# Performance work log

Hardware: AMD Instinct MI355X
Metric: run time of the kernel (lower is better)

Reference implementation:

```python
import jax, jax.numpy as jnp
import numpy as np

N_NODES = 100000
N_EDGES = 1600000
IN_CH = 128
OUT_CH = 128
BN_EPS = 1e-5


def setup_inputs() -> dict:
    key = jax.random.key(0)
    ks = jax.random.split(key, 8)
    x = jax.random.normal(ks[0], (N_NODES, IN_CH), dtype=jnp.float32)
    edge_index = jax.random.randint(ks[1], (2, N_EDGES), 0, N_NODES, dtype=jnp.int32)
    s1 = 1.0 / np.sqrt(IN_CH)
    s2 = 1.0 / np.sqrt(OUT_CH)
    W1 = jax.random.uniform(ks[2], (IN_CH, OUT_CH), minval=-s1, maxval=s1, dtype=jnp.float32)
    b1 = jax.random.uniform(ks[3], (OUT_CH,), minval=-s1, maxval=s1, dtype=jnp.float32)
    gamma = jnp.ones((OUT_CH,), dtype=jnp.float32)
    beta = jnp.zeros((OUT_CH,), dtype=jnp.float32)
    W2 = jax.random.uniform(ks[4], (OUT_CH, OUT_CH), minval=-s2, maxval=s2, dtype=jnp.float32)
    b2 = jax.random.uniform(ks[5], (OUT_CH,), minval=-s2, maxval=s2, dtype=jnp.float32)
    return {"x": x, "edge_index": edge_index, "W1": W1, "b1": b1,
            "gamma": gamma, "beta": beta, "W2": W2, "b2": b2}


def reference(x, edge_index, W1, b1, gamma, beta, W2, b2):
    # GINConv (eps=0): h_i = x_i + sum_{(j->i) in E} x_j
    src, dst = edge_index[0], edge_index[1]
    agg = jax.ops.segment_sum(x[src], dst, num_segments=N_NODES)  # [N, in_ch]
    h = x + agg
    # MLP: Linear -> BatchNorm1d (training-mode batch stats) -> ReLU -> Linear -> ReLU
    h = h @ W1 + b1                                   # [N, out_ch]
    mean = jnp.mean(h, axis=0)
    var = jnp.mean(jnp.square(h - mean), axis=0)      # biased variance, as in BN training
    h = (h - mean) * jax.lax.rsqrt(var + BN_EPS) * gamma + beta
    h = jax.nn.relu(h)
    h = h @ W2 + b2
    return jax.nn.relu(h)
```

## Files before the change

### kernel.cpp

```cpp
#include <hip/hip_runtime.h>
#include <hip/hip_bf16.h>
#include <hip/hip_fp16.h>
#include <stdint.h>

#define CH 128
#define NCHUNK 512
#define MAXBKT 2048

typedef _Float16 f16x8 __attribute__((ext_vector_type(8)));
typedef float f32x4 __attribute__((ext_vector_type(4)));

static __device__ __forceinline__ float4 ld4(const float* p) {
    return *reinterpret_cast<const float4*>(p);
}

__global__ void k_bhist(const int* __restrict__ dst, int* __restrict__ H,
                        int nE, int nbkt, int chunkSz) {
    __shared__ int hist[MAXBKT];
    int c = blockIdx.x, tid = threadIdx.x;
    for (int i = tid; i < nbkt; i += 256) hist[i] = 0;
    __syncthreads();
    int s = c * chunkSz, e = min(s + chunkSz, nE);
    for (int i = s + tid; i < e; i += 256) atomicAdd(&hist[dst[i] >> 6], 1);
    __syncthreads();
    for (int i = tid; i < nbkt; i += 256) H[c * nbkt + i] = hist[i];
}

__global__ void k_btot(const int* __restrict__ H, int* __restrict__ T, int nchunk, int nbkt) {
    __shared__ int sd[256];
    int b = blockIdx.x, tid = threadIdx.x;
    int v = 0;
    for (int c = tid; c < nchunk; c += 256) v += H[c * nbkt + b];
    sd[tid] = v;
    __syncthreads();
    for (int o = 128; o > 0; o >>= 1) {
        if (tid < o) sd[tid] += sd[tid + o];
        __syncthreads();
    }
    if (tid == 0) T[b] = sd[0];
}

__global__ __launch_bounds__(1024) void k_bscan(const int* __restrict__ T,
                                                int* __restrict__ base, int nbkt) {
    __shared__ int ps[1024];
    int t = threadIdx.x;
    int a0 = (2 * t < nbkt) ? T[2 * t] : 0;
    int a1 = (2 * t + 1 < nbkt) ? T[2 * t + 1] : 0;
    ps[t] = a0 + a1;
    __syncthreads();
    for (int d = 1; d < 1024; d <<= 1) {
        int v = (t >= d) ? ps[t - d] : 0;
        __syncthreads();
        ps[t] += v;
        __syncthreads();
    }
    int excl = t ? ps[t - 1] : 0;
    if (2 * t < nbkt) base[2 * t] = excl;
    if (2 * t + 1 < nbkt) base[2 * t + 1] = excl + a0;
    if (t == 0) base[nbkt] = ps[1023];
}

__global__ __launch_bounds__(512) void k_boff(int* H, const int* __restrict__ base,
                                              int nchunk, int nbkt) {
    __shared__ int sd[NCHUNK];
    int b = blockIdx.x, t = threadIdx.x;
    int v = (t < nchunk) ? H[t * nbkt + b] : 0;
    sd[t] = v;
    __syncthreads();
    for (int d = 1; d < NCHUNK; d <<= 1) {
        int tv = (t >= d) ? sd[t - d] : 0;
        __syncthreads();
        sd[t] += tv;
        __syncthreads();
    }
    if (t < nchunk) H[t * nbkt + b] = base[b] + sd[t] - v;
}

__global__ void k_bscatter(const int* __restrict__ src, const int* __restrict__ dst,
                           const int* __restrict__ H, int* __restrict__ sorted,
                           int nE, int nbkt, int chunkSz) {
    __shared__ int cur[MAXBKT];
    int c = blockIdx.x, tid = threadIdx.x;
    for (int i = tid; i < nbkt; i += 256) cur[i] = H[c * nbkt + i];
    __syncthreads();
    int s = c * chunkSz, e = min(s + chunkSz, nE);
    for (int i = s + tid; i < e; i += 256) {
        int d = dst[i];
        int pos = atomicAdd(&cur[d >> 6], 1);
        sorted[pos] = src[i] | ((d & 63) << 17);
    }
}

__global__ __launch_bounds__(256) void k_bsort2(const int* __restrict__ sorted,
        const int* __restrict__ base, int* __restrict__ csr, int* __restrict__ offs,
        int n, int nbkt, int nE) {
    __shared__ int hist[64];
    __shared__ int cur[64];
    int b = blockIdx.x, tid = threadIdx.x;
    if (tid < 64) hist[tid] = 0;
    __syncthreads();
    int s = base[b], e = base[b + 1];
    for (int i = s + tid; i < e; i += 256)
        atomicAdd(&hist[(sorted[i] >> 17) & 63], 1);
    __syncthreads();
    if (tid < 64) {
        int h0 = hist[tid];
        int v = h0;
        for (int d = 1; d < 64; d <<= 1) {
            int t = __shfl_up(v, d, 64);
            if (tid >= d) v += t;
        }
        int excl = base[b] + v - h0;
        int node = b * 64 + tid;
        if (node < n) offs[node] = excl;
        cur[tid] = excl;
    }
    if (b == 0 && tid == 0) offs[n] = nE;
    __syncthreads();
    for (int i = s + tid; i < e; i += 256) {
        int p = sorted[i];
        int pos = atomicAdd(&cur[(p >> 17) & 63], 1);
        csr[pos] = p & 0x1FFFF;
    }
}

__global__ void k_tofp16(const float* __restrict__ x, uint32_t* __restrict__ xh, int n8) {
    int i = blockIdx.x * blockDim.x + threadIdx.x;
    int st = gridDim.x * blockDim.x;
    for (; i < n8; i += st) {
        float4 v0 = ld4(x + (size_t)i * 8);
        float4 v1 = ld4(x + (size_t)i * 8 + 4);
        __half2 h0 = __floats2half2_rn(v0.x, v0.y);
        __half2 h1 = __floats2half2_rn(v0.z, v0.w);
        __half2 h2 = __floats2half2_rn(v1.x, v1.y);
        __half2 h3 = __floats2half2_rn(v1.z, v1.w);
        uint4 o;
        o.x = *reinterpret_cast<unsigned*>(&h0);
        o.y = *reinterpret_cast<unsigned*>(&h1);
        o.z = *reinterpret_cast<unsigned*>(&h2);
        o.w = *reinterpret_cast<unsigned*>(&h3);
        reinterpret_cast<uint4*>(xh)[i] = o;
    }
}

static __device__ __forceinline__ void acc4(float4& a, uint2 v) {
    __half2 p0 = *reinterpret_cast<__half2*>(&v.x);
    __half2 p1 = *reinterpret_cast<__half2*>(&v.y);
    float2 f0 = __half22float2(p0), f1 = __half22float2(p1);
    a.x += f0.x; a.y += f0.y; a.z += f1.x; a.w += f1.y;
}

__global__ void k_aggregate_h2(const uint2* __restrict__ xv,
        const int* __restrict__ csr, const int* __restrict__ offs,
        uint2* __restrict__ h16, int n) {
    int wid = (blockIdx.x * blockDim.x + threadIdx.x) >> 6;
    int lane = threadIdx.x & 63;
    int nw = (gridDim.x * blockDim.x) >> 6;
    int hf = lane >> 5;
    int l32 = lane & 31;
    for (int node = wid; node < n; node += nw) {
        float4 a0 = make_float4(0.f, 0.f, 0.f, 0.f), a1 = a0, a2 = a0, a3 = a0;
        if (hf == 0) acc4(a0, xv[(size_t)node * 32 + l32]);
        int s = offs[node], e = offs[node + 1];
        int i = s + hf;
        for (; i + 6 < e; i += 8) {
            int e0 = csr[i], e1 = csr[i + 2], e2 = csr[i + 4], e3 = csr[i + 6];
            uint2 v0 = xv[(size_t)e0 * 32 + l32];
            uint2 v1 = xv[(size_t)e1 * 32 + l32];
            uint2 v2 = xv[(size_t)e2 * 32 + l32];
            uint2 v3 = xv[(size_t)e3 * 32 + l32];
            acc4(a0, v0); acc4(a1, v1); acc4(a2, v2); acc4(a3, v3);
        }
        for (; i < e; i += 2)
            acc4(a0, xv[(size_t)csr[i] * 32 + l32]);
        a0.x += a1.x + a2.x + a3.x;
        a0.y += a1.y + a2.y + a3.y;
        a0.z += a1.z + a2.z + a3.z;
        a0.w += a1.w + a2.w + a3.w;
        a0.x += __shfl_xor(a0.x, 32, 64);
        a0.y += __shfl_xor(a0.y, 32, 64);
        a0.z += __shfl_xor(a0.z, 32, 64);
        a0.w += __shfl_xor(a0.w, 32, 64);
        if (hf == 0) {
            __half2 o0 = __floats2half2_rn(a0.x, a0.y);
            __half2 o1 = __floats2half2_rn(a0.z, a0.w);
            uint2 ov;
            ov.x = *reinterpret_cast<unsigned*>(&o0);
            ov.y = *reinterpret_cast<unsigned*>(&o1);
            h16[(size_t)node * 32 + l32] = ov;
        }
    }
}

__global__ __launch_bounds__(256) void k_mgemm(
        const _Float16* __restrict__ A, const float* __restrict__ W,
        const float* __restrict__ bias, _Float16* __restrict__ O16,
        float* __restrict__ O32, float* __restrict__ stats,
        const float* __restrict__ bnsc, int nrows, int doStats) {
    __shared__ _Float16 WT[CH * CH];
    __shared__ float sc_sh[2 * CH];
    int tid = threadIdx.x;
    for (int idx4 = tid * 4; idx4 < CH * CH; idx4 += 1024) {
        float4 wv = ld4(W + idx4);
        int k = idx4 >> 7, col = idx4 & 127;
        int s = k >> 3, j = k & 7;
#pragma unroll
        for (int q = 0; q < 4; ++q) {
            int c = col + q;
            WT[c * CH + ((s ^ (c & 7)) << 3) + j] =
                (_Float16)(q == 0 ? wv.x : q == 1 ? wv.y : q == 2 ? wv.z : wv.w);
        }
    }
    if (bnsc && tid < 2 * CH) sc_sh[tid] = bnsc[tid];
    __syncthreads();

    int wv = tid >> 6, lane = tid & 63;
    int lr = lane & 15;
    int lg = lane >> 4;

    float bv[8];
#pragma unroll
    for (int ct = 0; ct < 8; ++ct) bv[ct] = bias[ct * 16 + lr];
    float ssum[8], ssq[8];
#pragma unroll
    for (int ct = 0; ct < 8; ++ct) { ssum[ct] = 0.f; ssq[ct] = 0.f; }

    int nchunks = (nrows + 63) >> 6;
    for (int chunk = blockIdx.x; chunk < nchunks; chunk += gridDim.x) {
        int row0 = chunk * 64 + wv * 16;
        int arow = min(row0 + lr, nrows - 1);
        const _Float16* Ap = A + (size_t)arow * CH + lg * 8;
        f16x8 a[4];
#pragma unroll
        for (int kb = 0; kb < 4; ++kb)
            a[kb] = *reinterpret_cast<const f16x8*>(Ap + kb * 32);
        if (bnsc) {
#pragma unroll
            for (int kb = 0; kb < 4; ++kb) {
                int k0 = kb * 32 + lg * 8;
#pragma unroll
                for (int j = 0; j < 8; ++j) {
                    float f = (float)a[kb][j];
                    f = fmaxf(fmaf(f, sc_sh[k0 + j], sc_sh[CH + k0 + j]), 0.f);
                    a[kb][j] = (_Float16)f;
                }
            }
        }

        f32x4 acc[8];
#pragma unroll
        for (int ct = 0; ct < 8; ++ct) acc[ct] = (f32x4){0.f, 0.f, 0.f, 0.f};
#pragma unroll
        for (int ct = 0; ct < 8; ++ct) {
            int col = ct * 16 + lr;
            const _Float16* Wp = &WT[col * CH];
            int sw = (col & 7) << 3;
#pragma unroll
            for (int kb = 0; kb < 4; ++kb) {
                int s = kb * 4 + lg;
                f16x8 b = *reinterpret_cast<const f16x8*>(Wp + ((s << 3) ^ sw));
                acc[ct] = __builtin_amdgcn_mfma_f32_16x16x32_f16(a[kb], b, acc[ct], 0, 0, 0);
            }
        }

#pragma unroll
        for (int ct = 0; ct < 8; ++ct) {
            int col = ct * 16 + lr;
#pragma unroll
            for (int r = 0; r < 4; ++r) {
                int row = row0 + lg * 4 + r;
                if (row < nrows) {
                    float v = acc[ct][r] + bv[ct];
                    if (doStats) {
                        O16[(size_t)row * CH + col] = (_Float16)v;
                        ssum[ct] += v;
                        ssq[ct] += v * v;
                    } else {
                        O32[(size_t)row * CH + col] = fmaxf(v, 0.f);
                    }
                }
            }
        }
    }

    if (doStats) {
#pragma unroll
        for (int ct = 0; ct < 8; ++ct) {
            ssum[ct] += __shfl_xor(ssum[ct], 16, 64); ssum[ct] += __shfl_xor(ssum[ct], 32, 64);
            ssq[ct]  += __shfl_xor(ssq[ct], 16, 64);  ssq[ct]  += __shfl_xor(ssq[ct], 32, 64);
        }
        __syncthreads();
        float* red = (float*)WT;
        if (lg == 0) {
#pragma unroll
            for (int ct = 0; ct < 8; ++ct) {
                red[wv * 128 + ct * 16 + lr] = ssum[ct];
                red[512 + wv * 128 + ct * 16 + lr] = ssq[ct];
            }
        }
        __syncthreads();
        if (tid < 128) {
            float s = 0.f, q = 0.f;
#pragma unroll
            for (int w = 0; w < 4; ++w) { s += red[w * 128 + tid]; q += red[512 + w * 128 + tid]; }
            atomicAdd(&stats[tid], s);
            atomicAdd(&stats[128 + tid], q);
        }
    }
}

__global__ void k_bnfin(const float* __restrict__ stats, const float* __restrict__ gamma,
        const float* __restrict__ beta, float* __restrict__ scsh, float invN) {
    int c = threadIdx.x;
    if (c < CH) {
        float mean = stats[c] * invN;
        float var = stats[CH + c] * invN - mean * mean;
        float sc = gamma[c] * rsqrtf(var + 1e-5f);
        scsh[c] = sc;
        scsh[CH + c] = beta[c] - mean * sc;
    }
}

extern "C" void kernel_launch(void* const* d_in, const int* in_sizes, int n_in,
                              void* d_out, int out_size, void* d_ws, size_t ws_size,
                              hipStream_t stream) {
    const float* x     = (const float*)d_in[0];
    const int*   ei    = (const int*)d_in[1];
    const float* W1    = (const float*)d_in[2];
    const float* b1    = (const float*)d_in[3];
    const float* gamma = (const float*)d_in[4];
    const float* beta  = (const float*)d_in[5];
    const float* W2    = (const float*)d_in[6];
    const float* b2    = (const float*)d_in[7];

    const int N = in_sizes[0] / CH;
    const int E = in_sizes[1] / 2;
    const int* esrc = ei;
    const int* edst = ei + E;
    const int nbkt = (N + 63) >> 6;
    const int chunkSz = (E + NCHUNK - 1) / NCHUNK;

    int* H      = (int*)d_out;
    int* sorted = (int*)((char*)d_out + (((size_t)NCHUNK * nbkt * 4 + 255) & ~(size_t)255));
    _Float16* h16 = (_Float16*)d_out;

    char* w = (char*)d_ws;
    auto take = [&](size_t bytes) {
        char* p = w;
        w += (bytes + 255) & ~(size_t)255;
        return p;
    };
    int*      csr    = (int*)take((size_t)E * 4);
    int*      T      = (int*)take((size_t)(nbkt + 1) * 4);
    int*      base   = (int*)take((size_t)(nbkt + 1) * 4);
    int*      offs   = (int*)take((size_t)(N + 1) * 4);
    float*    stats  = (float*)take(256 * 4);
    float*    scsh   = (float*)take(256 * 4);
    uint32_t* xh     = (uint32_t*)take((size_t)N * CH * 2);
    _Float16* h1     = (_Float16*)xh;

    hipMemsetAsync(stats, 0, 256 * 4, stream);

    k_bhist<<<NCHUNK, 256, 0, stream>>>(edst, H, E, nbkt, chunkSz);
    k_btot<<<nbkt, 256, 0, stream>>>(H, T, NCHUNK, nbkt);
    k_bscan<<<1, 1024, 0, stream>>>(T, base, nbkt);
    k_boff<<<nbkt, NCHUNK, 0, stream>>>(H, base, NCHUNK, nbkt);
    k_bscatter<<<NCHUNK, 256, 0, stream>>>(esrc, edst, H, sorted, E, nbkt, chunkSz);
    k_bsort2<<<nbkt, 256, 0, stream>>>(sorted, base, csr, offs, N, nbkt, E);
    k_tofp16<<<2048, 256, 0, stream>>>(x, xh, N * CH / 8);
    k_aggregate_h2<<<4096, 256, 0, stream>>>((const uint2*)xh, csr, offs,
                                             (uint2*)h16, N);
    k_mgemm<<<512, 256, 0, stream>>>(h16, W1, b1, h1, nullptr, stats, nullptr, N, 1);
    k_bnfin<<<1, 128, 0, stream>>>(stats, gamma, beta, scsh, 1.0f / (float)N);
    k_mgemm<<<512, 256, 0, stream>>>(h1, W2, b2, nullptr, (float*)d_out, nullptr, scsh, N, 0);
}
```

Baseline: 210.1 us.

## Fuse CSR build and fp16 conversion into one cooperative kernel with grid syncs

Replaces the seven preprocessing launches (fp16 conversion, bucket histogram, totals, scan, offsets, scatter, local sort) with a single cooperative kernel that uses grid-wide syncs between phases, falling back to the separate launches if the cooperative launch fails. The BN finalize kernel is folded into the second GEMM's prologue, and the aggregation gains a 16-edge unrolled loop for more loads in flight. The aim is to cut launch overhead and inter-kernel gaps, at the cost of grid.sync barriers and a scan bucket phase now run by only 512 blocks in a grid-stride loop.

```diff
diff --git a/kernel.cpp b/kernel.cpp
--- a/kernel.cpp
+++ b/kernel.cpp
@@ -1,8 +1,11 @@
 #include <hip/hip_runtime.h>
+#include <hip/hip_cooperative_groups.h>
 #include <hip/hip_bf16.h>
 #include <hip/hip_fp16.h>
 #include <stdint.h>
 
+namespace cg = cooperative_groups;
+
 #define CH 128
 #define NCHUNK 512
 #define MAXBKT 2048
@@ -14,6 +17,149 @@
     return *reinterpret_cast<const float4*>(p);
 }
 
+static __device__ __forceinline__ void cvt_store_fp16(uint32_t* xh, int i, float4 v0, float4 v1) {
+    __half2 h0 = __floats2half2_rn(v0.x, v0.y);
+    __half2 h1 = __floats2half2_rn(v0.z, v0.w);
+    __half2 h2 = __floats2half2_rn(v1.x, v1.y);
+    __half2 h3 = __floats2half2_rn(v1.z, v1.w);
+    uint4 o;
+    o.x = *reinterpret_cast<unsigned*>(&h0);
+    o.y = *reinterpret_cast<unsigned*>(&h1);
+    o.z = *reinterpret_cast<unsigned*>(&h2);
+    o.w = *reinterpret_cast<unsigned*>(&h3);
+    reinterpret_cast<uint4*>(xh)[i] = o;
+}
+
+__global__ __launch_bounds__(256) void k_prep(const int* __restrict__ edst,
+        const int* __restrict__ esrc, const float* __restrict__ x,
+        uint32_t* __restrict__ xh, int* __restrict__ H, int* __restrict__ T,
+        int* __restrict__ base, int* __restrict__ sorted, int* __restrict__ csr,
+        int* __restrict__ offs, int n, int nE, int nbkt, int chunkSz, int n8) {
+    cg::grid_group grid = cg::this_grid();
+    __shared__ int smem[MAXBKT];
+    int tid = threadIdx.x, bid = blockIdx.x;
+    int gsz = gridDim.x * 256;
+    int gtid = bid * 256 + tid;
+
+    for (int i = gtid; i < n8; i += gsz)
+        cvt_store_fp16(xh, i, ld4(x + (size_t)i * 8), ld4(x + (size_t)i * 8 + 4));
+
+    for (int i = tid; i < nbkt; i += 256) smem[i] = 0;
+    __syncthreads();
+    int s = bid * chunkSz, e = min(s + chunkSz, nE);
+    for (int i = s + tid; i < e; i += 256) atomicAdd(&smem[edst[i] >> 6], 1);
+    __syncthreads();
+    for (int i = tid; i < nbkt; i += 256) H[bid * nbkt + i] = smem[i];
+    grid.sync();
+
+    for (int b = bid; b < nbkt; b += gridDim.x) {
+        __syncthreads();
+        int v = 0;
+        for (int c = tid; c < NCHUNK; c += 256) v += H[c * nbkt + b];
+        smem[tid] = v;
+        __syncthreads();
+        for (int o = 128; o > 0; o >>= 1) {
+            if (tid < o) smem[tid] += smem[tid + o];
+            __syncthreads();
+        }
+        if (tid == 0) T[b] = smem[0];
+    }
+    grid.sync();
+
+    if (bid == 0) {
+        __syncthreads();
+        int loc[8];
+        int tot = 0;
+#pragma unroll
+        for (int j = 0; j < 8; ++j) {
+            int idx = tid * 8 + j;
+            loc[j] = (idx < nbkt) ? T[idx] : 0;
+            tot += loc[j];
+        }
+        smem[tid] = tot;
+        __syncthreads();
+        for (int d = 1; d < 256; d <<= 1) {
+            int tv = (tid >= d) ? smem[tid - d] : 0;
+            __syncthreads();
+            smem[tid] += tv;
+            __syncthreads();
+        }
+        int run = smem[tid] - tot;
+#pragma unroll
+        for (int j = 0; j < 8; ++j) {
+            int idx = tid * 8 + j;
+            if (idx < nbkt) base[idx] = run;
+            run += loc[j];
+        }
+        if (tid == 255) base[nbkt] = smem[255];
+    }
+    grid.sync();
+
+    for (int b = bid; b < nbkt; b += gridDim.x) {
+        __syncthreads();
+        int c0 = 2 * tid, c1 = 2 * tid + 1;
+        int v0 = H[c0 * nbkt + b], v1 = H[c1 * nbkt + b];
+        smem[tid] = v0 + v1;
+        __syncthreads();
+        for (int d = 1; d < 256; d <<= 1) {
+            int tv = (tid >= d) ? smem[tid - d] : 0;
+            __syncthreads();
+            smem[tid] += tv;
+            __syncthreads();
+        }
+        int excl = base[b] + smem[tid] - (v0 + v1);
+        H[c0 * nbkt + b] = excl;
+        H[c1 * nbkt + b] = excl + v0;
+    }
+    grid.sync();
+
+    __syncthreads();
+    for (int i = tid; i < nbkt; i += 256) smem[i] = H[bid * nbkt + i];
+    __syncthreads();
+    for (int i = s + tid; i < e; i += 256) {
+        int d = edst[i];
+        int pos = atomicAdd(&smem[d >> 6], 1);
+        sorted[pos] = esrc[i] | ((d & 63) << 17);
+    }
+    grid.sync();
+
+    int* hist = smem;
+    int* cur = smem + 64;
+    for (int b = bid; b < nbkt; b += gridDim.x) {
+        __syncthreads();
+        if (tid < 64) hist[tid] = 0;
+        __syncthreads();
+        int bs = base[b], be = base[b + 1];
+        for (int i = bs + tid; i < be; i += 256)
+            atomicAdd(&hist[(sorted[i] >> 17) & 63], 1);
+        __syncthreads();
+        if (tid < 64) {
+            int h0 = hist[tid], v = h0;
+            for (int d = 1; d < 64; d <<= 1) {
+                int t = __shfl_up(v, d, 64);
+                if (tid >= d) v += t;
+            }
+            int excl = bs + v - h0;
+            int node = b * 64 + tid;
+            if (node < n) offs[node] = excl;
+            cur[tid] = excl;
+        }
+        __syncthreads();
+        for (int i = bs + tid; i < be; i += 256) {
+            int p = sorted[i];
+            int pos = atomicAdd(&cur[(p >> 17) & 63], 1);
+            csr[pos] = p & 0x1FFFF;
+        }
+    }
+    if (bid == 0 && tid == 0) offs[n] = nE;
+}
+
+__global__ void k_tofp16(const float* __restrict__ x, uint32_t* __restrict__ xh, int n8) {
+    int i = blockIdx.x * blockDim.x + threadIdx.x;
+    int st = gridDim.x * blockDim.x;
+    for (; i < n8; i += st)
+        cvt_store_fp16(xh, i, ld4(x + (size_t)i * 8), ld4(x + (size_t)i * 8 + 4));
+}
 __global__ void k_bhist(const int* __restrict__ dst, int* __restrict__ H,
                         int nE, int nbkt, int chunkSz) {
     __shared__ int hist[MAXBKT];
@@ -25,7 +171,6 @@
     __syncthreads();
     for (int i = tid; i < nbkt; i += 256) H[c * nbkt + i] = hist[i];
 }
-
 __global__ void k_btot(const int* __restrict__ H, int* __restrict__ T, int nchunk, int nbkt) {
     __shared__ int sd[256];
     int b = blockIdx.x, tid = threadIdx.x;
@@ -39,7 +184,6 @@
     }
     if (tid == 0) T[b] = sd[0];
 }
-
 __global__ __launch_bounds__(1024) void k_bscan(const int* __restrict__ T,
                                                 int* __restrict__ base, int nbkt) {
     __shared__ int ps[1024];
@@ -59,7 +203,6 @@
     if (2 * t + 1 < nbkt) base[2 * t + 1] = excl + a0;
     if (t == 0) base[nbkt] = ps[1023];
 }
-
 __global__ __launch_bounds__(512) void k_boff(int* H, const int* __restrict__ base,
                                               int nchunk, int nbkt) {
     __shared__ int sd[NCHUNK];
@@ -75,7 +218,6 @@
     }
     if (t < nchunk) H[t * nbkt + b] = base[b] + sd[t] - v;
 }
-
 __global__ void k_bscatter(const int* __restrict__ src, const int* __restrict__ dst,
                            const int* __restrict__ H, int* __restrict__ sorted,
                            int nE, int nbkt, int chunkSz) {
@@ -90,7 +232,6 @@
         sorted[pos] = src[i] | ((d & 63) << 17);
     }
 }
-
 __global__ __launch_bounds__(256) void k_bsort2(const int* __restrict__ sorted,
         const int* __restrict__ base, int* __restrict__ csr, int* __restrict__ offs,
         int n, int nbkt, int nE) {
@@ -104,8 +245,7 @@
         atomicAdd(&hist[(sorted[i] >> 17) & 63], 1);
     __syncthreads();
     if (tid < 64) {
-        int h0 = hist[tid];
-        int v = h0;
+        int h0 = hist[tid], v = h0;
         for (int d = 1; d < 64; d <<= 1) {
             int t = __shfl_up(v, d, 64);
             if (tid >= d) v += t;
@@ -121,25 +261,6 @@
         int p = sorted[i];
         int pos = atomicAdd(&cur[(p >> 17) & 63], 1);
         csr[pos] = p & 0x1FFFF;
-    }
-}
-
-__global__ void k_tofp16(const float* __restrict__ x, uint32_t* __restrict__ xh, int n8) {
-    int i = blockIdx.x * blockDim.x + threadIdx.x;
-    int st = gridDim.x * blockDim.x;
-    for (; i < n8; i += st) {
-        float4 v0 = ld4(x + (size_t)i * 8);
-        float4 v1 = ld4(x + (size_t)i * 8 + 4);
-        __half2 h0 = __floats2half2_rn(v0.x, v0.y);
-        __half2 h1 = __floats2half2_rn(v0.z, v0.w);
-        __half2 h2 = __floats2half2_rn(v1.x, v1.y);
-        __half2 h3 = __floats2half2_rn(v1.z, v1.w);
-        uint4 o;
-        o.x = *reinterpret_cast<unsigned*>(&h0);
-        o.y = *reinterpret_cast<unsigned*>(&h1);
-        o.z = *reinterpret_cast<unsigned*>(&h2);
-        o.w = *reinterpret_cast<unsigned*>(&h3);
-        reinterpret_cast<uint4*>(xh)[i] = o;
     }
 }
 
@@ -163,12 +284,23 @@
         if (hf == 0) acc4(a0, xv[(size_t)node * 32 + l32]);
         int s = offs[node], e = offs[node + 1];
         int i = s + hf;
+        for (; i + 14 < e; i += 16) {
+            uint2 v0 = xv[(size_t)csr[i]      * 32 + l32];
+            uint2 v1 = xv[(size_t)csr[i + 2]  * 32 + l32];
+            uint2 v2 = xv[(size_t)csr[i + 4]  * 32 + l32];
+            uint2 v3 = xv[(size_t)csr[i + 6]  * 32 + l32];
+            uint2 v4 = xv[(size_t)csr[i + 8]  * 32 + l32];
+            uint2 v5 = xv[(size_t)csr[i + 10] * 32 + l32];
+            uint2 v6 = xv[(size_t)csr[i + 12] * 32 + l32];
+            uint2 v7 = xv[(size_t)csr[i + 14] * 32 + l32];
+            acc4(a0, v0); acc4(a1, v1); acc4(a2, v2); acc4(a3, v3);
+            acc4(a0, v4); acc4(a1, v5); acc4(a2, v6); acc4(a3, v7);
+        }
         for (; i + 6 < e; i += 8) {
-            int e0 = csr[i], e1 = csr[i + 2], e2 = csr[i + 4], e3 = csr[i + 6];
-            uint2 v0 = xv[(size_t)e0 * 32 + l32];
-            uint2 v1 = xv[(size_t)e1 * 32 + l32];
-            uint2 v2 = xv[(size_t)e2 * 32 + l32];
-            uint2 v3 = xv[(size_t)e3 * 32 + l32];
+            uint2 v0 = xv[(size_t)csr[i]     * 32 + l32];
+            uint2 v1 = xv[(size_t)csr[i + 2] * 32 + l32];
+            uint2 v2 = xv[(size_t)csr[i + 4] * 32 + l32];
+            uint2 v3 = xv[(size_t)csr[i + 6] * 32 + l32];
             acc4(a0, v0); acc4(a1, v1); acc4(a2, v2); acc4(a3, v3);
         }
         for (; i < e; i += 2)
@@ -195,8 +327,9 @@
 __global__ __launch_bounds__(256) void k_mgemm(
         const _Float16* __restrict__ A, const float* __restrict__ W,
         const float* __restrict__ bias, _Float16* __restrict__ O16,
-        float* __restrict__ O32, float* __restrict__ stats,
-        const float* __restrict__ bnsc, int nrows, int doStats) {
+        float* __restrict__ O32, float* __restrict__ statsOut,
+        const float* __restrict__ statsIn, const float* __restrict__ gamma,
+        const float* __restrict__ beta, float invN, int nrows, int doStats) {
     __shared__ _Float16 WT[CH * CH];
     __shared__ float sc_sh[2 * CH];
     int tid = threadIdx.x;
@@ -211,7 +344,13 @@
                 (_Float16)(q == 0 ? wv.x : q == 1 ? wv.y : q == 2 ? wv.z : wv.w);
         }
     }
-    if (bnsc && tid < 2 * CH) sc_sh[tid] = bnsc[tid];
+    if (statsIn && tid < CH) {
+        float mean = statsIn[tid] * invN;
+        float var = statsIn[CH + tid] * invN - mean * mean;
+        float sc = gamma[tid] * rsqrtf(var + 1e-5f);
+        sc_sh[tid] = sc;
+        sc_sh[CH + tid] = beta[tid] - mean * sc;
+    }
     __syncthreads();
 
     int wv = tid >> 6, lane = tid & 63;
@@ -234,7 +373,7 @@
 #pragma unroll
         for (int kb = 0; kb < 4; ++kb)
             a[kb] = *reinterpret_cast<const f16x8*>(Ap + kb * 32);
-        if (bnsc) {
+        if (statsIn) {
 #pragma unroll
             for (int kb = 0; kb < 4; ++kb) {
                 int k0 = kb * 32 + lg * 8;
@@ -303,21 +442,9 @@
             float s = 0.f, q = 0.f;
 #pragma unroll
             for (int w = 0; w < 4; ++w) { s += red[w * 128 + tid]; q += red[512 + w * 128 + tid]; }
-            atomicAdd(&stats[tid], s);
-            atomicAdd(&stats[128 + tid], q);
-        }
-    }
-}
-
-__global__ void k_bnfin(const float* __restrict__ stats, const float* __restrict__ gamma,
-        const float* __restrict__ beta, float* __restrict__ scsh, float invN) {
-    int c = threadIdx.x;
-    if (c < CH) {
-        float mean = stats[c] * invN;
-        float var = stats[CH + c] * invN - mean * mean;
-        float sc = gamma[c] * rsqrtf(var + 1e-5f);
-        scsh[c] = sc;
-        scsh[CH + c] = beta[c] - mean * sc;
+            atomicAdd(&statsOut[tid], s);
+            atomicAdd(&statsOut[128 + tid], q);
+        }
     }
 }
 
@@ -333,12 +460,13 @@
     const float* W2    = (const float*)d_in[6];
     const float* b2    = (const float*)d_in[7];
 
-    const int N = in_sizes[0] / CH;
-    const int E = in_sizes[1] / 2;
+    int N = in_sizes[0] / CH;
+    int E = in_sizes[1] / 2;
     const int* esrc = ei;
     const int* edst = ei + E;
-    const int nbkt = (N + 63) >> 6;
-    const int chunkSz = (E + NCHUNK - 1) / NCHUNK;
+    int nbkt = (N + 63) >> 6;
+    int chunkSz = (E + NCHUNK - 1) / NCHUNK;
+    int n8 = N * CH / 8;
 
     int* H      = (int*)d_out;
     int* sorted = (int*)((char*)d_out + (((size_t)NCHUNK * nbkt * 4 + 255) & ~(size_t)255));
@@ -355,22 +483,35 @@
     int*      base   = (int*)take((size_t)(nbkt + 1) * 4);
     int*      offs   = (int*)take((size_t)(N + 1) * 4);
     float*    stats  = (float*)take(256 * 4);
-    float*    scsh   = (float*)take(256 * 4);
     uint32_t* xh     = (uint32_t*)take((size_t)N * CH * 2);
     _Float16* h1     = (_Float16*)xh;
 
     hipMemsetAsync(stats, 0, 256 * 4, stream);
 
-    k_bhist<<<NCHUNK, 256, 0, stream>>>(edst, H, E, nbkt, chunkSz);
-    k_btot<<<nbkt, 256, 0, stream>>>(H, T, NCHUNK, nbkt);
-    k_bscan<<<1, 1024, 0, stream>>>(T, base, nbkt);
-    k_boff<<<nbkt, NCHUNK, 0, stream>>>(H, base, NCHUNK, nbkt);
-    k_bscatter<<<NCHUNK, 256, 0, stream>>>(esrc, edst, H, sorted, E, nbkt, chunkSz);
-    k_bsort2<<<nbkt, 256, 0, stream>>>(sorted, base, csr, offs, N, nbkt, E);
-    k_tofp16<<<2048, 256, 0, stream>>>(x, xh, N * CH / 8);
+    {
+        const int* edst_ = edst;
+        const int* esrc_ = esrc;
+        const float* x_ = x;
+        void* args[] = {(void*)&edst_, (void*)&esrc_, (void*)&x_, (void*)&xh,
+                        (void*)&H, (void*)&T, (void*)&base, (void*)&sorted,
+                        (void*)&csr, (void*)&offs, (void*)&N, (void*)&E,
+                        (void*)&nbkt, (void*)&chunkSz, (void*)&n8};
+        hipError_t err = hipLaunchCooperativeKernel((void*)k_prep, dim3(NCHUNK), dim3(256),
+                                                    args, 0, stream);
+        if (err != hipSuccess) {
+            k_tofp16<<<2048, 256, 0, stream>>>(x, xh, n8);
+            k_bhist<<<NCHUNK, 256, 0, stream>>>(edst, H, E, nbkt, chunkSz);
+            k_btot<<<nbkt, 256, 0, stream>>>(H, T, NCHUNK, nbkt);
+            k_bscan<<<1, 1024, 0, stream>>>(T, base, nbkt);
+            k_boff<<<nbkt, NCHUNK, 0, stream>>>(H, base, NCHUNK, nbkt);
+            k_bscatter<<<NCHUNK, 256, 0, stream>>>(esrc, edst, H, sorted, E, nbkt, chunkSz);
+            k_bsort2<<<nbkt, 256, 0, stream>>>(sorted, base, csr, offs, N, nbkt, E);
+        }
+    }
     k_aggregate_h2<<<4096, 256, 0, stream>>>((const uint2*)xh, csr, offs,
                                              (uint2*)h16, N);
-    k_mgemm<<<512, 256, 0, stream>>>(h16, W1, b1, h1, nullptr, stats, nullptr, N, 1);
-    k_bnfin<<<1, 128, 0, stream>>>(stats, gamma, beta, scsh, 1.0f / (float)N);
-    k_mgemm<<<512, 256, 0, stream>>>(h1, W2, b2, nullptr, (float*)d_out, nullptr, scsh, N, 0);
-}
+    k_mgemm<<<512, 256, 0, stream>>>(h16, W1, b1, h1, nullptr, stats,
+                                     nullptr, nullptr, nullptr, 0.f, N, 1);
+    k_mgemm<<<512, 256, 0, stream>>>(h1, W2, b2, nullptr, (float*)d_out, nullptr,
+                                     stats, gamma, beta, 1.0f / (float)N, N, 0);
+}
```

Measured after the change: 494.0 us. 135% more time.
